# Kernel optimization log

Measured on AMD Instinct MI355X. Metric: run time of the kernel, lower is better.

The kernel has to match this reference:

```python
import jax, jax.numpy as jnp
import numpy as np
from jax import lax

B, L, C, H, W = 16, 8, 64, 50, 50
OC, K, PAD = 64, 3, 1
CQ = C // 16


def conv2d(x, w, b, pad):
    y = lax.conv_general_dilated(x, w, (1, 1), [(pad, pad), (pad, pad)],
                                 dimension_numbers=('NCHW', 'OIHW', 'NCHW'))
    return y + b[None, :, None, None]


def attention(x, y, q_w, q_b, k_w, k_b, v_w, v_b):
    # x, y: [b, C, 5, 5]
    b, c, h, w = x.shape
    q = conv2d(x, q_w, q_b, 1).reshape(b, -1, h * w)   # [b, CQ, N]
    kk = conv2d(y, k_w, k_b, 1).reshape(b, -1, h * w)  # [b, CQ, N]
    attn = jax.nn.softmax(jnp.einsum('bcn,bcm->bnm', q, kk), axis=-1)  # [b, Nq, Nk]
    v = conv2d(y, v_w, v_b, 1).reshape(b, c, h * w)    # [b, C, N]
    out = jnp.einsum('bcm,bnm->bcn', v, attn)          # bmm(V, attn^T)
    return out.reshape(b, c, h, w)


def setup_inputs():
    key = jax.random.key(0)
    ks = jax.random.split(key, 15)
    s = 0.05
    return {
        'x': jax.random.normal(ks[0], (B, L, C, H, W), jnp.float32),
        'weight': jax.random.normal(ks[1], (OC, C, K, K), jnp.float32) * s,
        'bias': jax.random.normal(ks[2], (OC,), jnp.float32) * s,
        'init_w': jax.random.normal(ks[3], (C, C, 3, 3), jnp.float32) * s,
        'init_b': jax.random.normal(ks[4], (C,), jnp.float32) * s,
        'q_w': jax.random.normal(ks[5], (CQ, C, 3, 3), jnp.float32) * s,
        'q_b': jax.random.normal(ks[6], (CQ,), jnp.float32) * s,
        'k_w': jax.random.normal(ks[7], (CQ, C, 3, 3), jnp.float32) * s,
        'k_b': jax.random.normal(ks[8], (CQ,), jnp.float32) * s,
        'v_w': jax.random.normal(ks[9], (C, C, 3, 3), jnp.float32) * s,
        'v_b': jax.random.normal(ks[10], (C,), jnp.float32) * s,
        'tconv_w': jax.random.normal(ks[11], (C, C), jnp.float32) * s,  # 1x1x1 Conv3d C->C
        'tconv_b': jax.random.normal(ks[12], (C,), jnp.float32) * s,
        'fc_w': jax.random.normal(ks[13], (C,), jnp.float32) * s,       # 1x1x1 Conv3d C->1
        'fc_b': jax.random.normal(ks[14], (), jnp.float32) * s,
    }


def reference(x, weight, bias, init_w, init_b, q_w, q_b, k_w, k_b, v_w, v_b,
              tconv_w, tconv_b, fc_w, fc_b):
    b, l, c, h, w = x.shape
    # --- generateweight ---
    xet = jnp.transpose(x, (0, 2, 1, 3, 4))  # [b, c, l, h, w]
    # AdaptiveMaxPool3d((None,5,5)); h,w multiples of 5 -> exact reshape max
    pooled = xet.reshape(b, c, l, 5, h // 5, 5, w // 5).max((4, 6))  # [b,c,l,5,5]
    seq = jnp.moveaxis(pooled, 2, 0)  # [l, b, c, 5, 5]
    prior0 = conv2d(seq[0], init_w, init_b, 1)

    def step(prior, xt):
        new = attention(prior, xt, q_w, q_b, k_w, k_b, v_w, v_b)
        return new, new

    _, allp = lax.scan(step, prior0, seq)            # [l, b, c, 5, 5]
    avg = jnp.moveaxis(allp, 0, 2).mean((3, 4))      # AdaptiveAvgPool3d -> [b, c, l]
    calib = jnp.einsum('oc,bcl->bol', tconv_w, avg) + tconv_b[None, :, None]  # [b,c,l]
    scale = 1.0 + jnp.transpose(calib, (0, 2, 1))    # [b, l, c]
    # finalweight[b,l,o,i,kh,kw] = weight[o,i,kh,kw] * scale[b,l,i]
    fw = weight[None, None] * scale[:, :, None, :, None, None]
    fc_out = jnp.einsum('c,bcl->bl', fc_w, avg) + fc_b  # [b, l]
    fb = bias[None, None, :] * (1.0 + fc_out)[:, :, None]  # [b, l, oc]
    # --- grouped conv with groups = b*l ---
    xg = x.reshape(1, b * l * c, h, w)
    wg = fw.reshape(b * l * OC, c, K, K)
    out = lax.conv_general_dilated(xg, wg, (1, 1), [(PAD, PAD), (PAD, PAD)],
                                   feature_group_count=b * l,
                                   dimension_numbers=('NCHW', 'OIHW', 'NCHW'))
    out = out.reshape(b * l, OC, out.shape[-2], out.shape[-1])
    out = out + fb.reshape(b * l, OC)[:, :, None, None]
    return out
```

## Files before the change

### kernel.cpp

```cpp
#include <hip/hip_runtime.h>

typedef short s16x8 __attribute__((ext_vector_type(8)));
typedef float f32x4 __attribute__((ext_vector_type(4)));

__device__ __forceinline__ unsigned short bf16r(float f) {
  unsigned int u = __float_as_uint(f);
  u += 0x7fffu + ((u >> 16) & 1u);
  return (unsigned short)(u >> 16);
}

__global__ __launch_bounds__(256) void pool_kernel(const float* __restrict__ x,
                                                   float* __restrict__ pooled) {
  const int blk = blockIdx.x;
  const float* plane = x + (size_t)blk * 2500;
  __shared__ float pmax[250];
  const int t = threadIdx.x;
  if (t < 250) {
    int r = t / 5, cc = t % 5;
    const float* row = plane + r * 50 + cc * 10;
    float m = row[0];
#pragma unroll
    for (int j = 1; j < 10; ++j) m = fmaxf(m, row[j]);
    pmax[r * 5 + cc] = m;
  }
  __syncthreads();
  if (t < 25) {
    int pr = t / 5, cc = t % 5;
    float m = pmax[(pr * 10) * 5 + cc];
#pragma unroll
    for (int rr = 1; rr < 10; ++rr) m = fmaxf(m, pmax[(pr * 10 + rr) * 5 + cc]);
    pooled[(size_t)blk * 25 + t] = m;
  }
}

__global__ __launch_bounds__(256) void wt_kernel(const float* __restrict__ w,
                                                 unsigned short* __restrict__ wt2) {
  int idx = blockIdx.x * 256 + threadIdx.x;
  if (idx >= 9 * 2 * 4 * 64 * 8) return;
  int j = idx & 7;
  int lane = (idx >> 3) & 63;
  int mf = (idx >> 9) & 3;
  int ik = (idx >> 11) & 1;
  int tap = idx >> 12;
  int o = mf * 16 + (lane & 15);
  int i = ik * 32 + 8 * (lane >> 4) + j;
  wt2[idx] = bf16r(w[((o * 64) + i) * 9 + tap]);
}

__device__ __forceinline__ void conv64(const float* pool_s, const float* __restrict__ wgt,
                                       const float* __restrict__ bias, float* red,
                                       float* __restrict__ outg, int tid) {
  int co = tid & 63, qd = tid >> 6;
  float acc[25];
#pragma unroll
  for (int n = 0; n < 25; ++n) acc[n] = 0.f;
  for (int ci = qd * 16; ci < qd * 16 + 16; ++ci) {
    float in[25];
#pragma unroll
    for (int n = 0; n < 25; ++n) in[n] = pool_s[ci * 25 + n];
    float w9[9];
#pragma unroll
    for (int tp = 0; tp < 9; ++tp) w9[tp] = wgt[(co * 64 + ci) * 9 + tp];
#pragma unroll
    for (int n = 0; n < 25; ++n) {
      int y = n / 5, xx = n % 5;
#pragma unroll
      for (int dy = 0; dy < 3; ++dy) {
        int yy = y + dy - 1;
        if (yy < 0 || yy > 4) continue;
#pragma unroll
        for (int dx = 0; dx < 3; ++dx) {
          int xc = xx + dx - 1;
          if (xc < 0 || xc > 4) continue;
          acc[n] += in[yy * 5 + xc] * w9[dy * 3 + dx];
        }
      }
    }
  }
#pragma unroll
  for (int n = 0; n < 25; ++n) red[(qd * 64 + co) * 25 + n] = acc[n];
  __syncthreads();
  for (int idx = tid; idx < 1600; idx += 256) {
    float s = red[idx] + red[1600 + idx] + red[3200 + idx] + red[4800 + idx];
    outg[idx] = s + bias[idx / 25];
  }
  __syncthreads();
}

__device__ __forceinline__ void conv4(const float* pool_s, const float* __restrict__ wgt,
                                      const float* __restrict__ bias, float* red,
                                      float* __restrict__ outg, int tid) {
  int co = tid & 3, ci = tid >> 2;
  float acc[25];
#pragma unroll
  for (int n = 0; n < 25; ++n) acc[n] = 0.f;
  float in[25];
#pragma unroll
  for (int n = 0; n < 25; ++n) in[n] = pool_s[ci * 25 + n];
  float w9[9];
#pragma unroll
  for (int tp = 0; tp < 9; ++tp) w9[tp] = wgt[(co * 64 + ci) * 9 + tp];
#pragma unroll
  for (int n = 0; n < 25; ++n) {
    int y = n / 5, xx = n % 5;
#pragma unroll
    for (int dy = 0; dy < 3; ++dy) {
      int yy = y + dy - 1;
      if (yy < 0 || yy > 4) continue;
#pragma unroll
      for (int dx = 0; dx < 3; ++dx) {
        int xc = xx + dx - 1;
        if (xc < 0 || xc > 4) continue;
        acc[n] += in[yy * 5 + xc] * w9[dy * 3 + dx];
      }
    }
  }
#pragma unroll
  for (int n = 0; n < 25; ++n) red[(ci * 4 + co) * 25 + n] = acc[n];
  __syncthreads();
  if (tid < 100) {
    int co2 = tid / 25, n = tid % 25;
    float s = 0.f;
    for (int c = 0; c < 64; ++c) s += red[(c * 4 + co2) * 25 + n];
    outg[co2 * 25 + n] = s + bias[co2];
  }
  __syncthreads();
}

__global__ __launch_bounds__(256) void convB_kernel(
    const float* __restrict__ pooled, const float* __restrict__ vw,
    const float* __restrict__ vb, const float* __restrict__ kw,
    const float* __restrict__ kb, const float* __restrict__ iw,
    const float* __restrict__ ib, float* __restrict__ vconv,
    float* __restrict__ kconv, float* __restrict__ prior0) {
  const int blk = blockIdx.x;
  __shared__ float pool_s[1600];
  __shared__ float red[6400];
  const int tid = threadIdx.x;
  for (int idx = tid; idx < 1600; idx += 256) pool_s[idx] = pooled[blk * 1600 + idx];
  __syncthreads();
  conv64(pool_s, vw, vb, red, vconv + blk * 1600, tid);
  conv4(pool_s, kw, kb, red, kconv + blk * 100, tid);
  if ((blk & 7) == 0) conv64(pool_s, iw, ib, red, prior0 + (blk >> 3) * 1600, tid);
}

__global__ __launch_bounds__(256) void scan_kernel(
    const float* __restrict__ vconv, const float* __restrict__ kconv,
    const float* __restrict__ prior0, const float* __restrict__ qw,
    const float* __restrict__ qb, const float* __restrict__ tconvw,
    const float* __restrict__ tconvb, const float* __restrict__ fcw,
    const float* __restrict__ fcb, const float* __restrict__ bias,
    float* __restrict__ scale_g, float* __restrict__ fb_g) {
  const int b = blockIdx.x;
  const int tid = threadIdx.x;
  __shared__ float p_s[1600], v_s[1600], kk_s[100], q_s[100];
  __shared__ float qw_s[2304];
  __shared__ float tcw_s[64 * 65];
  __shared__ float attn_s[625];
  __shared__ float red[6400];
  __shared__ float avg_s[64];

  for (int idx = tid; idx < 1600; idx += 256) p_s[idx] = prior0[b * 1600 + idx];
  for (int idx = tid; idx < 2304; idx += 256) qw_s[idx] = qw[idx];
  for (int idx = tid; idx < 4096; idx += 256) tcw_s[(idx / 64) * 65 + (idx % 64)] = tconvw[idx];
  __syncthreads();

  const int qco = tid & 3, qci = tid >> 2;
  float qwr[9];
#pragma unroll
  for (int tp = 0; tp < 9; ++tp) qwr[tp] = qw_s[(qco * 64 + qci) * 9 + tp];

  for (int l = 0; l < 8; ++l) {
    const int bl = b * 8 + l;
    for (int idx = tid; idx < 1600; idx += 256) v_s[idx] = vconv[bl * 1600 + idx];
    if (tid < 100) kk_s[tid] = kconv[bl * 100 + tid];
    __syncthreads();

    {
      float in[25];
#pragma unroll
      for (int n = 0; n < 25; ++n) in[n] = p_s[qci * 25 + n];
      float acc[25];
#pragma unroll
      for (int n = 0; n < 25; ++n) acc[n] = 0.f;
#pragma unroll
      for (int n = 0; n < 25; ++n) {
        int y = n / 5, xx = n % 5;
#pragma unroll
        for (int dy = 0; dy < 3; ++dy) {
          int yy = y + dy - 1;
          if (yy < 0 || yy > 4) continue;
#pragma unroll
          for (int dx = 0; dx < 3; ++dx) {
            int xc = xx + dx - 1;
            if (xc < 0 || xc > 4) continue;
            acc[n] += in[yy * 5 + xc] * qwr[dy * 3 + dx];
          }
        }
      }
#pragma unroll
      for (int n = 0; n < 25; ++n) red[(qci * 4 + qco) * 25 + n] = acc[n];
    }
    __syncthreads();
    if (tid < 100) {
      int co = tid / 25, n = tid % 25;
      float s = qb[co];
      for (int c = 0; c < 64; ++c) s += red[(c * 4 + co) * 25 + n];
      q_s[co * 25 + n] = s;
    }
    __syncthreads();
    for (int idx = tid; idx < 625; idx += 256) {
      int n = idx / 25, m = idx % 25;
      float s = 0.f;
#pragma unroll
      for (int c = 0; c < 4; ++c) s += q_s[c * 25 + n] * kk_s[c * 25 + m];
      attn_s[idx] = s;
    }
    __syncthreads();
    if (tid < 25) {
      float* row = attn_s + tid * 25;
      float mx = row[0];
#pragma unroll
      for (int m = 1; m < 25; ++m) mx = fmaxf(mx, row[m]);
      float sm = 0.f;
#pragma unroll
      for (int m = 0; m < 25; ++m) {
        float e = __expf(row[m] - mx);
        row[m] = e;
        sm += e;
      }
      float inv = 1.0f / sm;
#pragma unroll
      for (int m = 0; m < 25; ++m) row[m] *= inv;
    }
    __syncthreads();
    if (tid < 200) {
      int n = tid % 25, cc = tid / 25;
      float ar[25];
#pragma unroll
      for (int m = 0; m < 25; ++m) ar[m] = attn_s[n * 25 + m];
#pragma unroll
      for (int cj = 0; cj < 8; ++cj) {
        int c = cc * 8 + cj;
        float s = 0.f;
#pragma unroll
        for (int m = 0; m < 25; ++m) s += v_s[c * 25 + m] * ar[m];
        p_s[c * 25 + n] = s;
      }
    }
    __syncthreads();
    if (tid < 64) {
      float s = 0.f;
#pragma unroll
      for (int n = 0; n < 25; ++n) s += p_s[tid * 25 + n];
      avg_s[tid] = s * 0.04f;
    }
    __syncthreads();
    if (tid < 64) {
      int o = tid;
      float cal = tconvb[o];
      for (int c = 0; c < 64; ++c) cal += tcw_s[o * 65 + c] * avg_s[c];
      scale_g[bl * 64 + o] = 1.0f + cal;
      float part = fcw[o] * avg_s[o];
#pragma unroll
      for (int off = 32; off; off >>= 1) part += __shfl_down(part, off);
      float fc = __shfl(part, 0) + fcb[0];
      fb_g[bl * 64 + o] = bias[o] * (1.0f + fc);
    }
    __syncthreads();
  }
}

__global__ __launch_bounds__(256) void conv_main(
    const float* __restrict__ x, const unsigned short* __restrict__ wt2,
    const float* __restrict__ scale_g, const float* __restrict__ fb_g,
    float* __restrict__ out) {
  const int g = blockIdx.x & 127;
  const int band = blockIdx.x >> 7;
  const int y0 = band * 4;
  const int tid = threadIdx.x;
  __shared__ unsigned short in_s[6 * 66 * 64];
  __shared__ float scale_s[64], fb_s[64];
  if (tid < 64) {
    scale_s[tid] = scale_g[g * 64 + tid];
    fb_s[tid] = fb_g[g * 64 + tid];
  }
  __syncthreads();

  const float* xg = x + (size_t)g * 160000;
  for (int task = tid; task < 3168; task += 256) {
    int c = task % 66;
    int rc = task / 66;
    int r = rc >> 3;
    int chunk = rc & 7;
    int y = y0 - 1 + r;
    int xi = c - 1;
    unsigned int p0 = 0, p1 = 0, p2 = 0, p3 = 0;
    if (y >= 0 && y < 50 && xi >= 0 && xi < 50) {
      const float* px = xg + chunk * 8 * 2500 + y * 50 + xi;
      float f0 = px[0] * scale_s[chunk * 8 + 0];
      float f1 = px[2500] * scale_s[chunk * 8 + 1];
      float f2 = px[5000] * scale_s[chunk * 8 + 2];
      float f3 = px[7500] * scale_s[chunk * 8 + 3];
      float f4 = px[10000] * scale_s[chunk * 8 + 4];
      float f5 = px[12500] * scale_s[chunk * 8 + 5];
      float f6 = px[15000] * scale_s[chunk * 8 + 6];
      float f7 = px[17500] * scale_s[chunk * 8 + 7];
      p0 = (unsigned)bf16r(f0) | ((unsigned)bf16r(f1) << 16);
      p1 = (unsigned)bf16r(f2) | ((unsigned)bf16r(f3) << 16);
      p2 = (unsigned)bf16r(f4) | ((unsigned)bf16r(f5) << 16);
      p3 = (unsigned)bf16r(f6) | ((unsigned)bf16r(f7) << 16);
    }
    int chS = chunk ^ (c & 7);
    uint4* dst = (uint4*)&in_s[((r * 66 + c) << 6) + (chS << 3)];
    uint4 u4;
    u4.x = p0; u4.y = p1; u4.z = p2; u4.w = p3;
    *dst = u4;
  }
  __syncthreads();

  const int wave = tid >> 6, lane = tid & 63;
  const int l15 = lane & 15, l4 = lane >> 4;
  const int yrow = y0 + wave;
  if (yrow < 50) {
    f32x4 acc[4][4];
    f32x4 z = {0.f, 0.f, 0.f, 0.f};
#pragma unroll
    for (int mf = 0; mf < 4; ++mf)
#pragma unroll
      for (int nf = 0; nf < 4; ++nf) acc[mf][nf] = z;

#pragma unroll
    for (int dy = 0; dy < 3; ++dy) {
      const int rr = wave + dy;
#pragma unroll
      for (int dx = 0; dx < 3; ++dx) {
        const int tap = dy * 3 + dx;
#pragma unroll
        for (int ik = 0; ik < 2; ++ik) {
          s16x8 a[4], bfr[4];
#pragma unroll
          for (int mf = 0; mf < 4; ++mf)
            a[mf] = *reinterpret_cast<const s16x8*>(
                wt2 + ((((tap * 2 + ik) * 4 + mf) * 64 + lane) << 3));
#pragma unroll
          for (int nf = 0; nf < 4; ++nf) {
            int cc = nf * 16 + l15 + dx;
            int chS = (ik * 4 + l4) ^ (cc & 7);
            bfr[nf] = *reinterpret_cast<const s16x8*>(
                &in_s[((rr * 66 + cc) << 6) + (chS << 3)]);
          }
#pragma unroll
          for (int mf = 0; mf < 4; ++mf)
#pragma unroll
            for (int nf = 0; nf < 4; ++nf)
              acc[mf][nf] = __builtin_amdgcn_mfma_f32_16x16x32_bf16(
                  a[mf], bfr[nf], acc[mf][nf], 0, 0, 0);
        }
      }
    }
    float* og = out + (size_t)g * 64 * 2500 + yrow * 50;
#pragma unroll
    for (int mf = 0; mf < 4; ++mf) {
#pragma unroll
      for (int r = 0; r < 4; ++r) {
        int o = mf * 16 + l4 * 4 + r;
        float fbv = fb_s[o];
#pragma unroll
        for (int nf = 0; nf < 4; ++nf) {
          int xx = nf * 16 + l15;
          if (xx < 50) og[(size_t)o * 2500 + xx] = acc[mf][nf][r] + fbv;
        }
      }
    }
  }
}

extern "C" void kernel_launch(void* const* d_in, const int* in_sizes, int n_in,
                              void* d_out, int out_size, void* d_ws, size_t ws_size,
                              hipStream_t stream) {
  const float* x       = (const float*)d_in[0];
  const float* weight  = (const float*)d_in[1];
  const float* bias    = (const float*)d_in[2];
  const float* init_w  = (const float*)d_in[3];
  const float* init_b  = (const float*)d_in[4];
  const float* q_w     = (const float*)d_in[5];
  const float* q_b     = (const float*)d_in[6];
  const float* k_w     = (const float*)d_in[7];
  const float* k_b     = (const float*)d_in[8];
  const float* v_w     = (const float*)d_in[9];
  const float* v_b     = (const float*)d_in[10];
  const float* tconv_w = (const float*)d_in[11];
  const float* tconv_b = (const float*)d_in[12];
  const float* fc_w    = (const float*)d_in[13];
  const float* fc_b    = (const float*)d_in[14];
  float* out = (float*)d_out;

  float* ws = (float*)d_ws;
  float* pooled = ws;
  float* vconv  = ws + 204800;
  float* kconv  = ws + 409600;
  float* prior0 = ws + 422400;
  float* scaleg = ws + 448000;
  float* fbg    = ws + 456192;
  unsigned short* wt2 = (unsigned short*)(ws + 464384);

  pool_kernel<<<8192, 256, 0, stream>>>(x, pooled);
  wt_kernel<<<144, 256, 0, stream>>>(weight, wt2);
  convB_kernel<<<128, 256, 0, stream>>>(pooled, v_w, v_b, k_w, k_b, init_w, init_b,
                                        vconv, kconv, prior0);
  scan_kernel<<<16, 256, 0, stream>>>(vconv, kconv, prior0, q_w, q_b, tconv_w,
                                      tconv_b, fc_w, fc_b, bias, scaleg, fbg);
  conv_main<<<13 * 128, 256, 0, stream>>>(x, wt2, scaleg, fbg, out);
}
```

Before: 168.3 us.

## Fuse pooling with bf16 padded NHWC input prep and prescale weights per group

A new poolprep kernel reads x once to produce both the max-pooled features and a zero-padded, channel-last bf16 copy of the input. A wscale kernel folds the per-group scale into bf16 weights up front. The main conv can then stream tiles straight into LDS with global_load_lds, with no in-kernel conversion or scaling. This adds a large workspace buffer and an extra write and read of the bf16 input. A fallback keeps the old path when the workspace is too small.

After: 194.5 us. +15.6%, slower.

```diff
diff --git a/kernel.cpp b/kernel.cpp
--- a/kernel.cpp
+++ b/kernel.cpp
@@ -8,6 +8,189 @@
   u += 0x7fffu + ((u >> 16) & 1u);
   return (unsigned short)(u >> 16);
 }
+
+
+__global__ __launch_bounds__(256) void poolprep_kernel(
+    const float* __restrict__ x, float* __restrict__ pooled,
+    unsigned short* __restrict__ xs) {
+  const int blk = blockIdx.x;
+  const int g = blk / 5, band = blk % 5;
+  const float* xg = x + (size_t)g * 160000;
+  unsigned short* xsg = xs + (size_t)g * (52 * 52 * 64);
+  __shared__ float pm[64 * 10 * 5];
+  const int tid = threadIdx.x;
+
+  for (int task = tid; task < 2000; task += 256) {
+    int chunk = task & 7;
+    int rest = task >> 3;
+    int xpair = rest % 25;
+    int r = rest / 25;
+    int y = band * 10 + r;
+    const float* base = xg + (chunk * 8) * 2500 + y * 50 + xpair * 2;
+    float2 v[8];
+#pragma unroll
+    for (int k = 0; k < 8; ++k) v[k] = *(const float2*)(base + k * 2500);
+    uint4 a, b;
+    a.x = (unsigned)bf16r(v[0].x) | ((unsigned)bf16r(v[1].x) << 16);
+    a.y = (unsigned)bf16r(v[2].x) | ((unsigned)bf16r(v[3].x) << 16);
+    a.z = (unsigned)bf16r(v[4].x) | ((unsigned)bf16r(v[5].x) << 16);
+    a.w = (unsigned)bf16r(v[6].x) | ((unsigned)bf16r(v[7].x) << 16);
+    b.x = (unsigned)bf16r(v[0].y) | ((unsigned)bf16r(v[1].y) << 16);
+    b.y = (unsigned)bf16r(v[2].y) | ((unsigned)bf16r(v[3].y) << 16);
+    b.z = (unsigned)bf16r(v[4].y) | ((unsigned)bf16r(v[5].y) << 16);
+    b.w = (unsigned)bf16r(v[6].y) | ((unsigned)bf16r(v[7].y) << 16);
+    int xx = xpair * 2;
+    *(uint4*)&xsg[(((y + 1) * 52) + (xx + 1)) * 64 + chunk * 8] = a;
+    *(uint4*)&xsg[(((y + 1) * 52) + (xx + 2)) * 64 + chunk * 8] = b;
+  }
+  uint4 z4;
+  z4.x = 0; z4.y = 0; z4.z = 0; z4.w = 0;
+  for (int task = tid; task < 160; task += 256) {
+    int chunk = task & 7;
+    int rest = task >> 3;
+    int col = (rest & 1) ? 51 : 0;
+    int r = rest >> 1;
+    int y = band * 10 + r;
+    *(uint4*)&xsg[(((y + 1) * 52) + col) * 64 + chunk * 8] = z4;
+  }
+  if (band == 0) {
+    for (int task = tid; task < 416; task += 256)
+      *(uint4*)&xsg[(task >> 3) * 64 + (task & 7) * 8] = z4;
+  }
+  if (band == 4) {
+    for (int task = tid; task < 416; task += 256)
+      *(uint4*)&xsg[(51 * 52 + (task >> 3)) * 64 + (task & 7) * 8] = z4;
+  }
+
+  for (int task = tid; task < 640; task += 256) {
+    int r = task % 10;
+    int c = task / 10;
+    const float2* row = (const float2*)(xg + c * 2500 + (band * 10 + r) * 50);
+#pragma unroll
+    for (int ox = 0; ox < 5; ++ox) {
+      float2 v0 = row[ox * 5 + 0], v1 = row[ox * 5 + 1], v2 = row[ox * 5 + 2];
+      float2 v3 = row[ox * 5 + 3], v4 = row[ox * 5 + 4];
+      float m = fmaxf(fmaxf(fmaxf(v0.x, v0.y), fmaxf(v1.x, v1.y)),
+                      fmaxf(fmaxf(v2.x, v2.y), fmaxf(v3.x, v3.y)));
+      m = fmaxf(m, fmaxf(v4.x, v4.y));
+      pm[(c * 10 + r) * 5 + ox] = m;
+    }
+  }
+  __syncthreads();
+  for (int t2 = tid; t2 < 320; t2 += 256) {
+    int ox = t2 % 5, c = t2 / 5;
+    float m = pm[(c * 10) * 5 + ox];
+#pragma unroll
+    for (int r = 1; r < 10; ++r) m = fmaxf(m, pm[(c * 10 + r) * 5 + ox]);
+    pooled[(size_t)g * 1600 + c * 25 + band * 5 + ox] = m;
+  }
+}
+
+__global__ __launch_bounds__(256) void wscale_kernel(
+    const float* __restrict__ w, const float* __restrict__ scale_g,
+    unsigned short* __restrict__ wt3) {
+  const int g = blockIdx.x;
+  const int tid = threadIdx.x;
+  __shared__ float sc[64];
+  if (tid < 64) sc[tid] = scale_g[g * 64 + tid];
+  __syncthreads();
+  unsigned short* outg = wt3 + (size_t)g * 36864;
+  for (int idx = tid; idx < 36864; idx += 256) {
+    int j = idx & 7;
+    int lane = (idx >> 3) & 63;
+    int mf = (idx >> 9) & 3;
+    int ik = (idx >> 11) & 1;
+    int tap = idx >> 12;
+    int o = mf * 16 + (lane & 15);
+    int i = ik * 32 + 8 * (lane >> 4) + j;
+    outg[idx] = bf16r(w[((o * 64) + i) * 9 + tap] * sc[i]);
+  }
+}
+
+__global__ __launch_bounds__(256) void conv_main_fast(
+    const unsigned short* __restrict__ xs, const unsigned short* __restrict__ wt3,
+    const float* __restrict__ fb_g, float* __restrict__ out) {
+  const int g = blockIdx.x & 127;
+  const int band = blockIdx.x >> 7;
+  const int y0 = band * 4;
+  const int tid = threadIdx.x;
+  __shared__ unsigned short in_s[6 * 66 * 64];
+  __shared__ float fb_s[64];
+  if (tid < 64) fb_s[tid] = fb_g[g * 64 + tid];
+
+  const unsigned short* xsg = xs + (size_t)g * (52 * 52 * 64);
+  for (int task = tid; task < 3168; task += 256) {
+    int chunk = task & 7;
+    int c = (task >> 3) % 66;
+    int r = (task >> 3) / 66;
+    int py = y0 + r;
+    int srcChunk = chunk ^ (c & 7);
+    const unsigned short* src = xsg + ((size_t)(py * 52 + c) * 64 + srcChunk * 8);
+    unsigned short* ldsb = in_s + (size_t)(task & ~63) * 8;
+    __builtin_amdgcn_global_load_lds(
+        (const __attribute__((address_space(1))) void*)src,
+        (__attribute__((address_space(3))) void*)ldsb, 16, 0, 0);
+  }
+  __syncthreads();
+
+  const int wave = tid >> 6, lane = tid & 63;
+  const int l15 = lane & 15, l4 = lane >> 4;
+  const int yrow = y0 + wave;
+  if (yrow < 50) {
+    f32x4 acc[4][4];
+    f32x4 z = {0.f, 0.f, 0.f, 0.f};
+#pragma unroll
+    for (int mf = 0; mf < 4; ++mf)
+#pragma unroll
+      for (int nf = 0; nf < 4; ++nf) acc[mf][nf] = z;
+
+    const unsigned short* wg = wt3 + (size_t)g * 36864;
+#pragma unroll
+    for (int dy = 0; dy < 3; ++dy) {
+      const int rr = wave + dy;
+#pragma unroll
+      for (int dx = 0; dx < 3; ++dx) {
+        const int tap = dy * 3 + dx;
+#pragma unroll
+        for (int ik = 0; ik < 2; ++ik) {
+          s16x8 a[4], bfr[4];
+#pragma unroll
+          for (int mf = 0; mf < 4; ++mf)
+            a[mf] = *reinterpret_cast<const s16x8*>(
+                wg + ((((tap * 2 + ik) * 4 + mf) * 64 + lane) << 3));
+#pragma unroll
+          for (int nf = 0; nf < 4; ++nf) {
+            int cc = nf * 16 + l15 + dx;
+            int chS = (ik * 4 + l4) ^ (cc & 7);
+            bfr[nf] = *reinterpret_cast<const s16x8*>(
+                &in_s[((rr * 66 + cc) << 6) + (chS << 3)]);
+          }
+#pragma unroll
+          for (int mf = 0; mf < 4; ++mf)
+#pragma unroll
+            for (int nf = 0; nf < 4; ++nf)
+              acc[mf][nf] = __builtin_amdgcn_mfma_f32_16x16x32_bf16(
+                  a[mf], bfr[nf], acc[mf][nf], 0, 0, 0);
+        }
+      }
+    }
+    float* og = out + (size_t)g * 64 * 2500 + yrow * 50;
+#pragma unroll
+    for (int mf = 0; mf < 4; ++mf) {
+#pragma unroll
+      for (int r = 0; r < 4; ++r) {
+        int o = mf * 16 + l4 * 4 + r;
+        float fbv = fb_s[o];
+#pragma unroll
+        for (int nf = 0; nf < 4; ++nf) {
+          int xx = nf * 16 + l15;
+          if (xx < 50) og[(size_t)o * 2500 + xx] = acc[mf][nf][r] + fbv;
+        }
+      }
+    }
+  }
+}
+
 
 __global__ __launch_bounds__(256) void pool_kernel(const float* __restrict__ x,
                                                    float* __restrict__ pooled) {
@@ -36,7 +219,7 @@
 __global__ __launch_bounds__(256) void wt_kernel(const float* __restrict__ w,
                                                  unsigned short* __restrict__ wt2) {
   int idx = blockIdx.x * 256 + threadIdx.x;
-  if (idx >= 9 * 2 * 4 * 64 * 8) return;
+  if (idx >= 36864) return;
   int j = idx & 7;
   int lane = (idx >> 3) & 63;
   int mf = (idx >> 9) & 3;
@@ -45,230 +228,6 @@
   int o = mf * 16 + (lane & 15);
   int i = ik * 32 + 8 * (lane >> 4) + j;
   wt2[idx] = bf16r(w[((o * 64) + i) * 9 + tap]);
-}
-
-__device__ __forceinline__ void conv64(const float* pool_s, const float* __restrict__ wgt,
-                                       const float* __restrict__ bias, float* red,
-                                       float* __restrict__ outg, int tid) {
-  int co = tid & 63, qd = tid >> 6;
-  float acc[25];
-#pragma unroll
-  for (int n = 0; n < 25; ++n) acc[n] = 0.f;
-  for (int ci = qd * 16; ci < qd * 16 + 16; ++ci) {
-    float in[25];
-#pragma unroll
-    for (int n = 0; n < 25; ++n) in[n] = pool_s[ci * 25 + n];
-    float w9[9];
-#pragma unroll
-    for (int tp = 0; tp < 9; ++tp) w9[tp] = wgt[(co * 64 + ci) * 9 + tp];
-#pragma unroll
-    for (int n = 0; n < 25; ++n) {
-      int y = n / 5, xx = n % 5;
-#pragma unroll
-      for (int dy = 0; dy < 3; ++dy) {
-        int yy = y + dy - 1;
-        if (yy < 0 || yy > 4) continue;
-#pragma unroll
-        for (int dx = 0; dx < 3; ++dx) {
-          int xc = xx + dx - 1;
-          if (xc < 0 || xc > 4) continue;
-          acc[n] += in[yy * 5 + xc] * w9[dy * 3 + dx];
-        }
-      }
-    }
-  }
-#pragma unroll
-  for (int n = 0; n < 25; ++n) red[(qd * 64 + co) * 25 + n] = acc[n];
-  __syncthreads();
-  for (int idx = tid; idx < 1600; idx += 256) {
-    float s = red[idx] + red[1600 + idx] + red[3200 + idx] + red[4800 + idx];
-    outg[idx] = s + bias[idx / 25];
-  }
-  __syncthreads();
-}
-
-__device__ __forceinline__ void conv4(const float* pool_s, const float* __restrict__ wgt,
-                                      const float* __restrict__ bias, float* red,
-                                      float* __restrict__ outg, int tid) {
-  int co = tid & 3, ci = tid >> 2;
-  float acc[25];
-#pragma unroll
-  for (int n = 0; n < 25; ++n) acc[n] = 0.f;
-  float in[25];
-#pragma unroll
-  for (int n = 0; n < 25; ++n) in[n] = pool_s[ci * 25 + n];
-  float w9[9];
-#pragma unroll
-  for (int tp = 0; tp < 9; ++tp) w9[tp] = wgt[(co * 64 + ci) * 9 + tp];
-#pragma unroll
-  for (int n = 0; n < 25; ++n) {
-    int y = n / 5, xx = n % 5;
-#pragma unroll
-    for (int dy = 0; dy < 3; ++dy) {
-      int yy = y + dy - 1;
-      if (yy < 0 || yy > 4) continue;
-#pragma unroll
-      for (int dx = 0; dx < 3; ++dx) {
-        int xc = xx + dx - 1;
-        if (xc < 0 || xc > 4) continue;
-        acc[n] += in[yy * 5 + xc] * w9[dy * 3 + dx];
-      }
-    }
-  }
-#pragma unroll
-  for (int n = 0; n < 25; ++n) red[(ci * 4 + co) * 25 + n] = acc[n];
-  __syncthreads();
-  if (tid < 100) {
-    int co2 = tid / 25, n = tid % 25;
-    float s = 0.f;
-    for (int c = 0; c < 64; ++c) s += red[(c * 4 + co2) * 25 + n];
-    outg[co2 * 25 + n] = s + bias[co2];
-  }
-  __syncthreads();
-}
-
-__global__ __launch_bounds__(256) void convB_kernel(
-    const float* __restrict__ pooled, const float* __restrict__ vw,
-    const float* __restrict__ vb, const float* __restrict__ kw,
-    const float* __restrict__ kb, const float* __restrict__ iw,
-    const float* __restrict__ ib, float* __restrict__ vconv,
-    float* __restrict__ kconv, float* __restrict__ prior0) {
-  const int blk = blockIdx.x;
-  __shared__ float pool_s[1600];
-  __shared__ float red[6400];
-  const int tid = threadIdx.x;
-  for (int idx = tid; idx < 1600; idx += 256) pool_s[idx] = pooled[blk * 1600 + idx];
-  __syncthreads();
-  conv64(pool_s, vw, vb, red, vconv + blk * 1600, tid);
-  conv4(pool_s, kw, kb, red, kconv + blk * 100, tid);
-  if ((blk & 7) == 0) conv64(pool_s, iw, ib, red, prior0 + (blk >> 3) * 1600, tid);
-}
-
-__global__ __launch_bounds__(256) void scan_kernel(
-    const float* __restrict__ vconv, const float* __restrict__ kconv,
-    const float* __restrict__ prior0, const float* __restrict__ qw,
-    const float* __restrict__ qb, const float* __restrict__ tconvw,
-    const float* __restrict__ tconvb, const float* __restrict__ fcw,
-    const float* __restrict__ fcb, const float* __restrict__ bias,
-    float* __restrict__ scale_g, float* __restrict__ fb_g) {
-  const int b = blockIdx.x;
-  const int tid = threadIdx.x;
-  __shared__ float p_s[1600], v_s[1600], kk_s[100], q_s[100];
-  __shared__ float qw_s[2304];
-  __shared__ float tcw_s[64 * 65];
-  __shared__ float attn_s[625];
-  __shared__ float red[6400];
-  __shared__ float avg_s[64];
-
-  for (int idx = tid; idx < 1600; idx += 256) p_s[idx] = prior0[b * 1600 + idx];
-  for (int idx = tid; idx < 2304; idx += 256) qw_s[idx] = qw[idx];
-  for (int idx = tid; idx < 4096; idx += 256) tcw_s[(idx / 64) * 65 + (idx % 64)] = tconvw[idx];
-  __syncthreads();
-
-  const int qco = tid & 3, qci = tid >> 2;
-  float qwr[9];
-#pragma unroll
-  for (int tp = 0; tp < 9; ++tp) qwr[tp] = qw_s[(qco * 64 + qci) * 9 + tp];
-
-  for (int l = 0; l < 8; ++l) {
-    const int bl = b * 8 + l;
-    for (int idx = tid; idx < 1600; idx += 256) v_s[idx] = vconv[bl * 1600 + idx];
-    if (tid < 100) kk_s[tid] = kconv[bl * 100 + tid];
-    __syncthreads();
-
-    {
-      float in[25];
-#pragma unroll
-      for (int n = 0; n < 25; ++n) in[n] = p_s[qci * 25 + n];
-      float acc[25];
-#pragma unroll
-      for (int n = 0; n < 25; ++n) acc[n] = 0.f;
-#pragma unroll
-      for (int n = 0; n < 25; ++n) {
-        int y = n / 5, xx = n % 5;
-#pragma unroll
-        for (int dy = 0; dy < 3; ++dy) {
-          int yy = y + dy - 1;
-          if (yy < 0 || yy > 4) continue;
-#pragma unroll
-          for (int dx = 0; dx < 3; ++dx) {
-            int xc = xx + dx - 1;
-            if (xc < 0 || xc > 4) continue;
-            acc[n] += in[yy * 5 + xc] * qwr[dy * 3 + dx];
-          }
-        }
-      }
-#pragma unroll
-      for (int n = 0; n < 25; ++n) red[(qci * 4 + qco) * 25 + n] = acc[n];
-    }
-    __syncthreads();
-    if (tid < 100) {
-      int co = tid / 25, n = tid % 25;
-      float s = qb[co];
-      for (int c = 0; c < 64; ++c) s += red[(c * 4 + co) * 25 + n];
-      q_s[co * 25 + n] = s;
-    }
-    __syncthreads();
-    for (int idx = tid; idx < 625; idx += 256) {
-      int n = idx / 25, m = idx % 25;
-      float s = 0.f;
-#pragma unroll
-      for (int c = 0; c < 4; ++c) s += q_s[c * 25 + n] * kk_s[c * 25 + m];
-      attn_s[idx] = s;
-    }
-    __syncthreads();
-    if (tid < 25) {
-      float* row = attn_s + tid * 25;
-      float mx = row[0];
-#pragma unroll
-      for (int m = 1; m < 25; ++m) mx = fmaxf(mx, row[m]);
-      float sm = 0.f;
-#pragma unroll
-      for (int m = 0; m < 25; ++m) {
-        float e = __expf(row[m] - mx);
-        row[m] = e;
-        sm += e;
-      }
-      float inv = 1.0f / sm;
-#pragma unroll
-      for (int m = 0; m < 25; ++m) row[m] *= inv;
-    }
-    __syncthreads();
-    if (tid < 200) {
-      int n = tid % 25, cc = tid / 25;
-      float ar[25];
-#pragma unroll
-      for (int m = 0; m < 25; ++m) ar[m] = attn_s[n * 25 + m];
-#pragma unroll
-      for (int cj = 0; cj < 8; ++cj) {
-        int c = cc * 8 + cj;
-        float s = 0.f;
-#pragma unroll
-        for (int m = 0; m < 25; ++m) s += v_s[c * 25 + m] * ar[m];
-        p_s[c * 25 + n] = s;
-      }
-    }
-    __syncthreads();
-    if (tid < 64) {
-      float s = 0.f;
-#pragma unroll
-      for (int n = 0; n < 25; ++n) s += p_s[tid * 25 + n];
-      avg_s[tid] = s * 0.04f;
-    }
-    __syncthreads();
-    if (tid < 64) {
-      int o = tid;
-      float cal = tconvb[o];
-      for (int c = 0; c < 64; ++c) cal += tcw_s[o * 65 + c] * avg_s[c];
-      scale_g[bl * 64 + o] = 1.0f + cal;
-      float part = fcw[o] * avg_s[o];
-#pragma unroll
-      for (int off = 32; off; off >>= 1) part += __shfl_down(part, off);
-      float fc = __shfl(part, 0) + fcb[0];
-      fb_g[bl * 64 + o] = bias[o] * (1.0f + fc);
-    }
-    __syncthreads();
-  }
 }
 
 __global__ __launch_bounds__(256) void conv_main(
@@ -286,7 +245,6 @@
     fb_s[tid] = fb_g[g * 64 + tid];
   }
   __syncthreads();
-
   const float* xg = x + (size_t)g * 160000;
   for (int task = tid; task < 3168; task += 256) {
     int c = task % 66;
@@ -318,7 +276,6 @@
     *dst = u4;
   }
   __syncthreads();
-
   const int wave = tid >> 6, lane = tid & 63;
   const int l15 = lane & 15, l4 = lane >> 4;
   const int yrow = y0 + wave;
@@ -329,7 +286,6 @@
     for (int mf = 0; mf < 4; ++mf)
 #pragma unroll
       for (int nf = 0; nf < 4; ++nf) acc[mf][nf] = z;
-
 #pragma unroll
     for (int dy = 0; dy < 3; ++dy) {
       const int rr = wave + dy;
@@ -373,6 +329,230 @@
         }
       }
     }
+  }
+}
+
+
+__device__ __forceinline__ void conv64(const float* pool_s, const float* __restrict__ wgt,
+                                       const float* __restrict__ bias, float* red,
+                                       float* __restrict__ outg, int tid) {
+  int co = tid & 63, qd = tid >> 6;
+  float acc[25];
+#pragma unroll
+  for (int n = 0; n < 25; ++n) acc[n] = 0.f;
+  for (int ci = qd * 16; ci < qd * 16 + 16; ++ci) {
+    float in[25];
+#pragma unroll
+    for (int n = 0; n < 25; ++n) in[n] = pool_s[ci * 25 + n];
+    float w9[9];
+#pragma unroll
+    for (int tp = 0; tp < 9; ++tp) w9[tp] = wgt[(co * 64 + ci) * 9 + tp];
+#pragma unroll
+    for (int n = 0; n < 25; ++n) {
+      int y = n / 5, xx = n % 5;
+#pragma unroll
+      for (int dy = 0; dy < 3; ++dy) {
+        int yy = y + dy - 1;
+        if (yy < 0 || yy > 4) continue;
+#pragma unroll
+        for (int dx = 0; dx < 3; ++dx) {
+          int xc = xx + dx - 1;
+          if (xc < 0 || xc > 4) continue;
+          acc[n] += in[yy * 5 + xc] * w9[dy * 3 + dx];
+        }
+      }
+    }
+  }
+#pragma unroll
+  for (int n = 0; n < 25; ++n) red[(qd * 64 + co) * 25 + n] = acc[n];
+  __syncthreads();
+  for (int idx = tid; idx < 1600; idx += 256) {
+    float s = red[idx] + red[1600 + idx] + red[3200 + idx] + red[4800 + idx];
+    outg[idx] = s + bias[idx / 25];
+  }
+  __syncthreads();
+}
+
+__device__ __forceinline__ void conv4(const float* pool_s, const float* __restrict__ wgt,
+                                      const float* __restrict__ bias, float* red,
+                                      float* __restrict__ outg, int tid) {
+  int co = tid & 3, ci = tid >> 2;
+  float acc[25];
+#pragma unroll
+  for (int n = 0; n < 25; ++n) acc[n] = 0.f;
+  float in[25];
+#pragma unroll
+  for (int n = 0; n < 25; ++n) in[n] = pool_s[ci * 25 + n];
+  float w9[9];
+#pragma unroll
+  for (int tp = 0; tp < 9; ++tp) w9[tp] = wgt[(co * 64 + ci) * 9 + tp];
+#pragma unroll
+  for (int n = 0; n < 25; ++n) {
+    int y = n / 5, xx = n % 5;
+#pragma unroll
+    for (int dy = 0; dy < 3; ++dy) {
+      int yy = y + dy - 1;
+      if (yy < 0 || yy > 4) continue;
+#pragma unroll
+      for (int dx = 0; dx < 3; ++dx) {
+        int xc = xx + dx - 1;
+        if (xc < 0 || xc > 4) continue;
+        acc[n] += in[yy * 5 + xc] * w9[dy * 3 + dx];
+      }
+    }
+  }
+#pragma unroll
+  for (int n = 0; n < 25; ++n) red[(ci * 4 + co) * 25 + n] = acc[n];
+  __syncthreads();
+  if (tid < 100) {
+    int co2 = tid / 25, n = tid % 25;
+    float s = 0.f;
+    for (int c = 0; c < 64; ++c) s += red[(c * 4 + co2) * 25 + n];
+    outg[co2 * 25 + n] = s + bias[co2];
+  }
+  __syncthreads();
+}
+
+__global__ __launch_bounds__(256) void convB_kernel(
+    const float* __restrict__ pooled, const float* __restrict__ vw,
+    const float* __restrict__ vb, const float* __restrict__ kw,
+    const float* __restrict__ kb, const float* __restrict__ iw,
+    const float* __restrict__ ib, float* __restrict__ vconv,
+    float* __restrict__ kconv, float* __restrict__ prior0) {
+  const int blk = blockIdx.x;
+  __shared__ float pool_s[1600];
+  __shared__ float red[6400];
+  const int tid = threadIdx.x;
+  for (int idx = tid; idx < 1600; idx += 256) pool_s[idx] = pooled[blk * 1600 + idx];
+  __syncthreads();
+  conv64(pool_s, vw, vb, red, vconv + blk * 1600, tid);
+  conv4(pool_s, kw, kb, red, kconv + blk * 100, tid);
+  if ((blk & 7) == 0) conv64(pool_s, iw, ib, red, prior0 + (blk >> 3) * 1600, tid);
+}
+
+__global__ __launch_bounds__(256) void scan_kernel(
+    const float* __restrict__ vconv, const float* __restrict__ kconv,
+    const float* __restrict__ prior0, const float* __restrict__ qw,
+    const float* __restrict__ qb, const float* __restrict__ tconvw,
+    const float* __restrict__ tconvb, const float* __restrict__ fcw,
+    const float* __restrict__ fcb, const float* __restrict__ bias,
+    float* __restrict__ scale_g, float* __restrict__ fb_g) {
+  const int b = blockIdx.x;
+  const int tid = threadIdx.x;
+  __shared__ float p_s[1600], v_s[1600], kk_s[100], q_s[100];
+  __shared__ float qw_s[2304];
+  __shared__ float tcw_s[64 * 65];
+  __shared__ float attn_s[625];
+  __shared__ float red[6400];
+  __shared__ float avg_s[64];
+
+  for (int idx = tid; idx < 1600; idx += 256) p_s[idx] = prior0[b * 1600 + idx];
+  for (int idx = tid; idx < 2304; idx += 256) qw_s[idx] = qw[idx];
+  for (int idx = tid; idx < 4096; idx += 256) tcw_s[(idx / 64) * 65 + (idx % 64)] = tconvw[idx];
+  __syncthreads();
+
+  const int qco = tid & 3, qci = tid >> 2;
+  float qwr[9];
+#pragma unroll
+  for (int tp = 0; tp < 9; ++tp) qwr[tp] = qw_s[(qco * 64 + qci) * 9 + tp];
+
+  for (int l = 0; l < 8; ++l) {
+    const int bl = b * 8 + l;
+    for (int idx = tid; idx < 1600; idx += 256) v_s[idx] = vconv[bl * 1600 + idx];
+    if (tid < 100) kk_s[tid] = kconv[bl * 100 + tid];
+    __syncthreads();
+    {
+      float in[25];
+#pragma unroll
+      for (int n = 0; n < 25; ++n) in[n] = p_s[qci * 25 + n];
+      float acc[25];
+#pragma unroll
+      for (int n = 0; n < 25; ++n) acc[n] = 0.f;
+#pragma unroll
+      for (int n = 0; n < 25; ++n) {
+        int y = n / 5, xx = n % 5;
+#pragma unroll
+        for (int dy = 0; dy < 3; ++dy) {
+          int yy = y + dy - 1;
+          if (yy < 0 || yy > 4) continue;
+#pragma unroll
+          for (int dx = 0; dx < 3; ++dx) {
+            int xc = xx + dx - 1;
+            if (xc < 0 || xc > 4) continue;
+            acc[n] += in[yy * 5 + xc] * qwr[dy * 3 + dx];
+          }
+        }
+      }
+#pragma unroll
+      for (int n = 0; n < 25; ++n) red[(qci * 4 + qco) * 25 + n] = acc[n];
+    }
+    __syncthreads();
+    if (tid < 100) {
+      int co = tid / 25, n = tid % 25;
+      float s = qb[co];
+      for (int c = 0; c < 64; ++c) s += red[(c * 4 + co) * 25 + n];
+      q_s[co * 25 + n] = s;
+    }
+    __syncthreads();
+    for (int idx = tid; idx < 625; idx += 256) {
+      int n = idx / 25, m = idx % 25;
+      float s = 0.f;
+#pragma unroll
+      for (int c = 0; c < 4; ++c) s += q_s[c * 25 + n] * kk_s[c * 25 + m];
+      attn_s[idx] = s;
+    }
+    __syncthreads();
+    if (tid < 25) {
+      float* row = attn_s + tid * 25;
+      float mx = row[0];
+#pragma unroll
+      for (int m = 1; m < 25; ++m) mx = fmaxf(mx, row[m]);
+      float sm = 0.f;
+#pragma unroll
+      for (int m = 0; m < 25; ++m) {
+        float e = __expf(row[m] - mx);
+        row[m] = e;
+        sm += e;
+      }
+      float inv = 1.0f / sm;
+#pragma unroll
+      for (int m = 0; m < 25; ++m) row[m] *= inv;
+    }
+    __syncthreads();
+    if (tid < 200) {
+      int n = tid % 25, cc = tid / 25;
+      float ar[25];
+#pragma unroll
+      for (int m = 0; m < 25; ++m) ar[m] = attn_s[n * 25 + m];
+#pragma unroll
+      for (int cj = 0; cj < 8; ++cj) {
+        int c = cc * 8 + cj;
+        float s = 0.f;
+#pragma unroll
+        for (int m = 0; m < 25; ++m) s += v_s[c * 25 + m] * ar[m];
+        p_s[c * 25 + n] = s;
+      }
+    }
+    __syncthreads();
+    if (tid < 64) {
+      float s = 0.f;
+#pragma unroll
+      for (int n = 0; n < 25; ++n) s += p_s[tid * 25 + n];
+      avg_s[tid] = s * 0.04f;
+    }
+    __syncthreads();
+    if (tid < 64) {
+      int o = tid;
+      float cal = tconvb[o];
+      for (int c = 0; c < 64; ++c) cal += tcw_s[o * 65 + c] * avg_s[c];
+      scale_g[bl * 64 + o] = 1.0f + cal;
+      float part = fcw[o] * avg_s[o];
+#pragma unroll
+      for (int off = 32; off; off >>= 1) part += __shfl_down(part, off);
+      float fc = __shfl(part, 0) + fcb[0];
+      fb_g[bl * 64 + o] = bias[o] * (1.0f + fc);
+    }
+    __syncthreads();
   }
 }
 
@@ -403,13 +583,27 @@
   float* prior0 = ws + 422400;
   float* scaleg = ws + 448000;
   float* fbg    = ws + 456192;
-  unsigned short* wt2 = (unsigned short*)(ws + 464384);
-
-  pool_kernel<<<8192, 256, 0, stream>>>(x, pooled);
-  wt_kernel<<<144, 256, 0, stream>>>(weight, wt2);
-  convB_kernel<<<128, 256, 0, stream>>>(pooled, v_w, v_b, k_w, k_b, init_w, init_b,
-                                        vconv, kconv, prior0);
-  scan_kernel<<<16, 256, 0, stream>>>(vconv, kconv, prior0, q_w, q_b, tconv_w,
-                                      tconv_b, fc_w, fc_b, bias, scaleg, fbg);
-  conv_main<<<13 * 128, 256, 0, stream>>>(x, wt2, scaleg, fbg, out);
-}
+  unsigned short* wt3 = (unsigned short*)(ws + 464384);
+  unsigned short* xsb = wt3 + 4718592;
+
+  const size_t NEED_FAST = 55662592ull;
+
+  if (ws_size >= NEED_FAST) {
+    poolprep_kernel<<<640, 256, 0, stream>>>(x, pooled, xsb);
+    convB_kernel<<<128, 256, 0, stream>>>(pooled, v_w, v_b, k_w, k_b, init_w, init_b,
+                                          vconv, kconv, prior0);
+    scan_kernel<<<16, 256, 0, stream>>>(vconv, kconv, prior0, q_w, q_b, tconv_w,
+                                        tconv_b, fc_w, fc_b, bias, scaleg, fbg);
+    wscale_kernel<<<128, 256, 0, stream>>>(weight, scaleg, wt3);
+    conv_main_fast<<<13 * 128, 256, 0, stream>>>(xsb, wt3, fbg, out);
+  } else {
+    unsigned short* wt2 = (unsigned short*)(ws + 464384);
+    pool_kernel<<<8192, 256, 0, stream>>>(x, pooled);
+    wt_kernel<<<144, 256, 0, stream>>>(weight, wt2);
+    convB_kernel<<<128, 256, 0, stream>>>(pooled, v_w, v_b, k_w, k_b, init_w, init_b,
+                                          vconv, kconv, prior0);
+    scan_kernel<<<16, 256, 0, stream>>>(vconv, kconv, prior0, q_w, q_b, tconv_w,
+                                        tconv_b, fc_w, fc_b, bias, scaleg, fbg);
+    conv_main<<<13 * 128, 256, 0, stream>>>(x, wt2, scaleg, fbg, out);
+  }
+}
```
